# Optimization experiments

Measured on AMD Instinct MI355X. Metric: run time of the kernel, lower is better.

## Reference

```python
import jax, jax.numpy as jnp
import numpy as np


def setup_inputs() -> dict:
    key = jax.random.key(0)
    k1, k2 = jax.random.split(key)
    pred_corners = jax.random.normal(k1, (2048, 8, 3), dtype=jnp.float32)
    gt_corners = jax.random.normal(k2, (2048, 8, 3), dtype=jnp.float32)
    return {"pred_corners": pred_corners, "gt_corners": gt_corners}


def _chamfer(pred_corners, gt_corners):
    # flatten boxes -> point clouds: [Np*8, 3], [Ng*8, 3]
    x = pred_corners.reshape(-1, 3)
    y = gt_corners.reshape(-1, 3)
    x2 = jnp.sum(x * x, axis=-1)  # [N]
    y2 = jnp.sum(y * y, axis=-1)  # [M]
    d2 = x2[:, None] + y2[None, :] - 2.0 * jnp.einsum("nd,md->nm", x, y)
    dist = jnp.sqrt(jnp.maximum(d2, 0.0))  # [N, M]
    # bidirectional min, averaged per box (8 corners) then over boxes
    min_p2g = jnp.min(dist, axis=1).reshape(-1, 8).mean(axis=1)
    min_g2p = jnp.min(dist, axis=0).reshape(-1, 8).mean(axis=1)
    return min_p2g.mean() + min_g2p.mean()


def reference(pred_corners, gt_corners):
    return _chamfer(pred_corners, gt_corners)
```

## Files before the change

kernel.cpp:

```cpp
#include <hip/hip_runtime.h>


#define NPTS   16384
#define BLOCKB 512
#define WAVES  8
#define XT_W   8
#define XPB    (WAVES * XT_W * 16)
#define NXB    (NPTS / XPB)
#define NYCH   16
#define YCH    (NPTS / NYCH)
#define SUBT   8
#define SUBPTS (SUBT * 16)
#define NSUB   (YCH / SUBPTS)
#define ONEBF  0x3F80

#define WS_PGB (1u << 20)
#define WS_PGA (2u << 20)
#define WS_PPB (3u << 20)
#define WS_PART (4u << 20)

typedef __attribute__((ext_vector_type(8))) short bf16x8;
typedef __attribute__((ext_vector_type(4))) float f32x4;

__device__ inline unsigned short f2bf(float f) {
    unsigned int u = __float_as_uint(f);
    return (unsigned short)((u + 0x7FFFu + ((u >> 16) & 1u)) >> 16);
}
__device__ inline float bf2f(unsigned short h) {
    return __uint_as_float((unsigned int)h << 16);
}
__device__ inline void split3(float v, unsigned short* s) {
    unsigned short h = f2bf(v);  float r = v - bf2f(h);
    unsigned short m = f2bf(r);  r -= bf2f(m);
    s[0] = h; s[1] = m; s[2] = f2bf(r);
}

__device__ inline void build_rows(const float p[3], unsigned short* a,
                                  unsigned short* b) {
    const int CI[6] = {0, 0, 1, 0, 1, 2};
    const int CJ[6] = {0, 1, 0, 2, 1, 0};
    unsigned short xs[3][3], nn[3], t[3];
#pragma unroll
    for (int d = 0; d < 3; ++d) {
        split3(p[d], t);
        xs[0][d] = t[0]; xs[1][d] = t[1]; xs[2][d] = t[2];
    }
    split3(-0.5f * (p[0]*p[0] + p[1]*p[1] + p[2]*p[2]), nn);
#pragma unroll
    for (int c = 0; c < 6; ++c)
#pragma unroll
        for (int d = 0; d < 3; ++d) {
            a[c*3+d] = xs[CI[c]][d];
            b[c*3+d] = xs[CJ[c]][d];
        }
#pragma unroll
    for (int k = 0; k < 3; ++k) {
        a[18+k] = nn[k];  b[18+k] = ONEBF;
        a[21+k] = ONEBF;  b[21+k] = nn[k];
    }
#pragma unroll
    for (int k = 24; k < 32; ++k) { a[k] = 0; b[k] = 0; }
}

__device__ inline void store_row(unsigned short* dst, const unsigned short* s) {
    unsigned int w[16];
#pragma unroll
    for (int k = 0; k < 16; ++k)
        w[k] = (unsigned int)s[2*k] | ((unsigned int)s[2*k+1] << 16);
    uint4* d4 = reinterpret_cast<uint4*>(dst);
#pragma unroll
    for (int k = 0; k < 4; ++k)
        d4[k] = make_uint4(w[4*k], w[4*k+1], w[4*k+2], w[4*k+3]);
}

__global__ __launch_bounds__(256) void pack_points(
        const float* __restrict__ pred, const float* __restrict__ gt,
        unsigned short* __restrict__ Ppa, unsigned short* __restrict__ Pgb,
        unsigned short* __restrict__ Pga, unsigned short* __restrict__ Ppb) {
    const int i = blockIdx.x * 256 + threadIdx.x;
    if (i >= NPTS) return;
    float p[3] = {pred[3*i], pred[3*i+1], pred[3*i+2]};
    float q[3] = {gt[3*i],   gt[3*i+1],   gt[3*i+2]};
    unsigned short ra[32], rb[32];
    build_rows(p, ra, rb);
    store_row(Ppa + (size_t)i * 32, ra);
    store_row(Ppb + (size_t)i * 32, rb);
    build_rows(q, ra, rb);
    store_row(Pga + (size_t)i * 32, ra);
    store_row(Pgb + (size_t)i * 32, rb);
}

template <int CTRL>
__device__ inline float rormax(float v) {
    int t = __builtin_amdgcn_update_dpp(0, __float_as_int(v), CTRL, 0xF, 0xF,
                                        false);
    return fmaxf(v, __int_as_float(t));
}

__global__ __launch_bounds__(BLOCKB, 4) void chamfer_part(
        const unsigned short* __restrict__ Ppa,
        const unsigned short* __restrict__ Pgb,
        const unsigned short* __restrict__ Pga,
        const unsigned short* __restrict__ Ppb,
        float* __restrict__ part) {
    const int xb  = blockIdx.x;
    const int yc  = blockIdx.y;
    const int dir = blockIdx.z;
    const unsigned short* __restrict__ Ap = dir ? Pga : Ppa;
    const unsigned short* __restrict__ Bp = dir ? Ppb : Pgb;
    const int tid = threadIdx.x;
    const int lane = tid & 63, w = tid >> 6;
    const int col = lane & 15, kg = lane >> 4;

    __shared__ __align__(16) char lbuf[2][SUBT * 16 * 64];

    const int xt0 = xb * (WAVES * XT_W) + w * XT_W;
    bf16x8 af[XT_W];
#pragma unroll
    for (int xi = 0; xi < XT_W; ++xi)
        af[xi] = *reinterpret_cast<const bf16x8*>(
            Ap + (size_t)((xt0 + xi) * 16 + col) * 32 + kg * 8);

    f32x4 rmax[XT_W];
#pragma unroll
    for (int xi = 0; xi < XT_W; ++xi)
        rmax[xi] = (f32x4){-3.0e38f, -3.0e38f, -3.0e38f, -3.0e38f};

    const f32x4 z4 = {0.0f, 0.0f, 0.0f, 0.0f};
    const char* ysrc = reinterpret_cast<const char*>(Bp) + (size_t)yc * YCH * 64;

    uint4 ld = *reinterpret_cast<const uint4*>(ysrc + tid * 16);
#pragma unroll 1
    for (int sc = 0; sc < NSUB; ++sc) {
        __syncthreads();
        *reinterpret_cast<uint4*>(&lbuf[sc & 1][tid * 16]) = ld;
        if (sc + 1 < NSUB)
            ld = *reinterpret_cast<const uint4*>(
                ysrc + (size_t)(sc + 1) * (SUBPTS * 64) + tid * 16);
        __syncthreads();
        const char* buf = lbuf[sc & 1];
#pragma unroll
        for (int t = 0; t < SUBT; t += 2) {
            bf16x8 b0 = *reinterpret_cast<const bf16x8*>(
                buf + ((t + 0) * 16 + col) * 64 + kg * 16);
            bf16x8 b1 = *reinterpret_cast<const bf16x8*>(
                buf + ((t + 1) * 16 + col) * 64 + kg * 16);
#pragma unroll
            for (int xi = 0; xi < XT_W; ++xi) {
                f32x4 A = __builtin_amdgcn_mfma_f32_16x16x32_bf16(af[xi], b0, z4, 0, 0, 0);
                f32x4 B = __builtin_amdgcn_mfma_f32_16x16x32_bf16(af[xi], b1, z4, 0, 0, 0);
                rmax[xi].x = fmaxf(fmaxf(A.x, B.x), rmax[xi].x);
                rmax[xi].y = fmaxf(fmaxf(A.y, B.y), rmax[xi].y);
                rmax[xi].z = fmaxf(fmaxf(A.z, B.z), rmax[xi].z);
                rmax[xi].w = fmaxf(fmaxf(A.w, B.w), rmax[xi].w);
            }
        }
    }

    float* pslice = part + (size_t)(dir * NYCH + yc) * NPTS;
#pragma unroll
    for (int xi = 0; xi < XT_W; ++xi) {
#define FLUSH(R, COMP)                                                        \
        {                                                                     \
            float v = rmax[xi].COMP;                                          \
            v = rormax<0x121>(v);                                             \
            v = rormax<0x122>(v);                                             \
            v = rormax<0x124>(v);                                             \
            v = rormax<0x128>(v);                                             \
            if (col == 0) {                                                   \
                float d2 = fmaxf(-2.0f * v, 0.0f);           \
                pslice[(xt0 + xi) * 16 + kg * 4 + R] = d2;                    \
            }                                                                 \
        }
        FLUSH(0, x) FLUSH(1, y) FLUSH(2, z) FLUSH(3, w)
#undef FLUSH
    }
}

__global__ __launch_bounds__(256) void chamfer_reduce(
        const float* __restrict__ part, float* __restrict__ out) {
    const int gid = blockIdx.x * 256 + threadIdx.x;
    const int dir = gid >> 14, x = gid & (NPTS - 1);
    float m = 3.0e38f;
#pragma unroll
    for (int c = 0; c < NYCH; ++c)
        m = fminf(m, part[(size_t)(dir * NYCH + c) * NPTS + x]);
    float s = sqrtf(m);
#pragma unroll
    for (int off = 32; off > 0; off >>= 1)
        s += __shfl_down(s, off, 64);
    if ((threadIdx.x & 63) == 0)
        atomicAdd(out, s * (1.0f / (float)NPTS));
}

extern "C" void kernel_launch(void* const* d_in, const int* in_sizes, int n_in,
                              void* d_out, int out_size, void* d_ws, size_t ws_size,
                              hipStream_t stream) {
    const float* pred = (const float*)d_in[0];
    const float* gt   = (const float*)d_in[1];
    float* out        = (float*)d_out;
    unsigned short* Ppa = (unsigned short*)d_ws;
    unsigned short* Pgb = (unsigned short*)((char*)d_ws + WS_PGB);
    unsigned short* Pga = (unsigned short*)((char*)d_ws + WS_PGA);
    unsigned short* Ppb = (unsigned short*)((char*)d_ws + WS_PPB);
    float* part         = (float*)((char*)d_ws + WS_PART);

    hipMemsetAsync(d_out, 0, sizeof(float), stream);
    hipLaunchKernelGGL(pack_points, dim3(NPTS / 256), dim3(256), 0, stream,
                       pred, gt, Ppa, Pgb, Pga, Ppb);
    hipLaunchKernelGGL(chamfer_part, dim3(NXB, NYCH, 2), dim3(BLOCKB), 0, stream,
                       Ppa, Pgb, Pga, Ppb, part);
    hipLaunchKernelGGL(chamfer_reduce, dim3(2 * NPTS / 256), dim3(256), 0, stream,
                       part, out);
}
```

Before: 97.02 us.

## Compute both chamfer directions from one distance matrix pass

```diff
diff --git a/kernel.cpp b/kernel.cpp
--- a/kernel.cpp
+++ b/kernel.cpp
@@ -2,22 +2,16 @@
 
 
 #define NPTS   16384
-#define BLOCKB 512
-#define WAVES  8
-#define XT_W   8
-#define XPB    (WAVES * XT_W * 16)
-#define NXB    (NPTS / XPB)
-#define NYCH   16
-#define YCH    (NPTS / NYCH)
-#define SUBT   8
-#define SUBPTS (SUBT * 16)
-#define NSUB   (YCH / SUBPTS)
+#define BLOCK  256
+#define XCH    256
+#define NXC    (NPTS / XCH)
+#define YCH    1024
+#define NYC    (NPTS / YCH)
+#define YW     256
 #define ONEBF  0x3F80
 
-#define WS_PGB (1u << 20)
-#define WS_PGA (2u << 20)
-#define WS_PPB (3u << 20)
-#define WS_PART (4u << 20)
+#define WS_PGB  (1u << 20)
+#define WS_PART (2u << 20)
 
 typedef __attribute__((ext_vector_type(8))) short bf16x8;
 typedef __attribute__((ext_vector_type(4))) float f32x4;
@@ -75,8 +69,7 @@
 
 __global__ __launch_bounds__(256) void pack_points(
         const float* __restrict__ pred, const float* __restrict__ gt,
-        unsigned short* __restrict__ Ppa, unsigned short* __restrict__ Pgb,
-        unsigned short* __restrict__ Pga, unsigned short* __restrict__ Ppb) {
+        unsigned short* __restrict__ Ppa, unsigned short* __restrict__ Pgb) {
     const int i = blockIdx.x * 256 + threadIdx.x;
     if (i >= NPTS) return;
     float p[3] = {pred[3*i], pred[3*i+1], pred[3*i+2]};
@@ -84,9 +77,7 @@
     unsigned short ra[32], rb[32];
     build_rows(p, ra, rb);
     store_row(Ppa + (size_t)i * 32, ra);
-    store_row(Ppb + (size_t)i * 32, rb);
     build_rows(q, ra, rb);
-    store_row(Pga + (size_t)i * 32, ra);
     store_row(Pgb + (size_t)i * 32, rb);
 }
 
@@ -97,94 +88,87 @@
     return fmaxf(v, __int_as_float(t));
 }
 
-__global__ __launch_bounds__(BLOCKB, 4) void chamfer_part(
+__global__ __launch_bounds__(BLOCK, 4) void chamfer_bidi(
         const unsigned short* __restrict__ Ppa,
         const unsigned short* __restrict__ Pgb,
-        const unsigned short* __restrict__ Pga,
-        const unsigned short* __restrict__ Ppb,
         float* __restrict__ part) {
-    const int xb  = blockIdx.x;
-    const int yc  = blockIdx.y;
-    const int dir = blockIdx.z;
-    const unsigned short* __restrict__ Ap = dir ? Pga : Ppa;
-    const unsigned short* __restrict__ Bp = dir ? Ppb : Pgb;
-    const int tid = threadIdx.x;
-    const int lane = tid & 63, w = tid >> 6;
+    const int xb = blockIdx.x, yc = blockIdx.y;
+    const int lane = threadIdx.x & 63, w = threadIdx.x >> 6;
     const int col = lane & 15, kg = lane >> 4;
+    const int xbase = xb * XCH;
+    const int ybase = yc * YCH + w * YW;
 
-    __shared__ __align__(16) char lbuf[2][SUBT * 16 * 64];
+    float* __restrict__ rowp = part + (size_t)(yc * 4 + w) * NPTS;
+    float* __restrict__ colp = part + (size_t)(64 + xb) * NPTS;
 
-    const int xt0 = xb * (WAVES * XT_W) + w * XT_W;
-    bf16x8 af[XT_W];
+    bf16x8 bfr[16];
 #pragma unroll
-    for (int xi = 0; xi < XT_W; ++xi)
-        af[xi] = *reinterpret_cast<const bf16x8*>(
-            Ap + (size_t)((xt0 + xi) * 16 + col) * 32 + kg * 8);
+    for (int yt = 0; yt < 16; ++yt)
+        bfr[yt] = *reinterpret_cast<const bf16x8*>(
+            Pgb + (size_t)(ybase + yt * 16 + col) * 32 + kg * 8);
 
-    f32x4 rmax[XT_W];
+    float cmax[16];
 #pragma unroll
-    for (int xi = 0; xi < XT_W; ++xi)
-        rmax[xi] = (f32x4){-3.0e38f, -3.0e38f, -3.0e38f, -3.0e38f};
+    for (int yt = 0; yt < 16; ++yt) cmax[yt] = -3.0e38f;
 
     const f32x4 z4 = {0.0f, 0.0f, 0.0f, 0.0f};
-    const char* ysrc = reinterpret_cast<const char*>(Bp) + (size_t)yc * YCH * 64;
 
-    uint4 ld = *reinterpret_cast<const uint4*>(ysrc + tid * 16);
+    bf16x8 afn = *reinterpret_cast<const bf16x8*>(
+        Ppa + (size_t)(xbase + col) * 32 + kg * 8);
+
 #pragma unroll 1
-    for (int sc = 0; sc < NSUB; ++sc) {
-        __syncthreads();
-        *reinterpret_cast<uint4*>(&lbuf[sc & 1][tid * 16]) = ld;
-        if (sc + 1 < NSUB)
-            ld = *reinterpret_cast<const uint4*>(
-                ysrc + (size_t)(sc + 1) * (SUBPTS * 64) + tid * 16);
-        __syncthreads();
-        const char* buf = lbuf[sc & 1];
+    for (int xt = 0; xt < 16; ++xt) {
+        bf16x8 afc = afn;
+        afn = *reinterpret_cast<const bf16x8*>(
+            Ppa + (size_t)(xbase + (((xt + 1) & 15) * 16) + col) * 32 + kg * 8);
+
+        f32x4 rmax = {-3.0e38f, -3.0e38f, -3.0e38f, -3.0e38f};
 #pragma unroll
-        for (int t = 0; t < SUBT; t += 2) {
-            bf16x8 b0 = *reinterpret_cast<const bf16x8*>(
-                buf + ((t + 0) * 16 + col) * 64 + kg * 16);
-            bf16x8 b1 = *reinterpret_cast<const bf16x8*>(
-                buf + ((t + 1) * 16 + col) * 64 + kg * 16);
+        for (int yt = 0; yt < 16; yt += 2) {
+            f32x4 A = __builtin_amdgcn_mfma_f32_16x16x32_bf16(afc, bfr[yt],     z4, 0, 0, 0);
+            f32x4 B = __builtin_amdgcn_mfma_f32_16x16x32_bf16(afc, bfr[yt + 1], z4, 0, 0, 0);
+            rmax.x = fmaxf(fmaxf(A.x, B.x), rmax.x);
+            rmax.y = fmaxf(fmaxf(A.y, B.y), rmax.y);
+            rmax.z = fmaxf(fmaxf(A.z, B.z), rmax.z);
+            rmax.w = fmaxf(fmaxf(A.w, B.w), rmax.w);
+            float ta = fmaxf(fmaxf(A.x, A.y), A.z);
+            cmax[yt]     = fmaxf(fmaxf(ta, A.w), cmax[yt]);
+            float tb = fmaxf(fmaxf(B.x, B.y), B.z);
+            cmax[yt + 1] = fmaxf(fmaxf(tb, B.w), cmax[yt + 1]);
+        }
+
 #pragma unroll
-            for (int xi = 0; xi < XT_W; ++xi) {
-                f32x4 A = __builtin_amdgcn_mfma_f32_16x16x32_bf16(af[xi], b0, z4, 0, 0, 0);
-                f32x4 B = __builtin_amdgcn_mfma_f32_16x16x32_bf16(af[xi], b1, z4, 0, 0, 0);
-                rmax[xi].x = fmaxf(fmaxf(A.x, B.x), rmax[xi].x);
-                rmax[xi].y = fmaxf(fmaxf(A.y, B.y), rmax[xi].y);
-                rmax[xi].z = fmaxf(fmaxf(A.z, B.z), rmax[xi].z);
-                rmax[xi].w = fmaxf(fmaxf(A.w, B.w), rmax[xi].w);
-            }
+        for (int i = 0; i < 4; ++i) {
+            float v = rmax[i];
+            v = rormax<0x121>(v);
+            v = rormax<0x122>(v);
+            v = rormax<0x124>(v);
+            v = rormax<0x128>(v);
+            if (col == 0)
+                rowp[xbase + xt * 16 + kg * 4 + i] =
+                    fmaxf(-2.0f * v, 0.0f);
         }
     }
 
-    float* pslice = part + (size_t)(dir * NYCH + yc) * NPTS;
 #pragma unroll
-    for (int xi = 0; xi < XT_W; ++xi) {
-#define FLUSH(R, COMP)                                                        \
-        {                                                                     \
-            float v = rmax[xi].COMP;                                          \
-            v = rormax<0x121>(v);                                             \
-            v = rormax<0x122>(v);                                             \
-            v = rormax<0x124>(v);                                             \
-            v = rormax<0x128>(v);                                             \
-            if (col == 0) {                                                   \
-                float d2 = fmaxf(-2.0f * v, 0.0f);           \
-                pslice[(xt0 + xi) * 16 + kg * 4 + R] = d2;                    \
-            }                                                                 \
-        }
-        FLUSH(0, x) FLUSH(1, y) FLUSH(2, z) FLUSH(3, w)
-#undef FLUSH
+    for (int yt = 0; yt < 16; ++yt) {
+        float v = cmax[yt];
+        v = fmaxf(v, __shfl_xor(v, 16, 64));
+        v = fmaxf(v, __shfl_xor(v, 32, 64));
+        if (kg == 0)
+            colp[ybase + yt * 16 + col] = fmaxf(-2.0f * v, 0.0f);
     }
 }
 
 __global__ __launch_bounds__(256) void chamfer_reduce(
         const float* __restrict__ part, float* __restrict__ out) {
     const int gid = blockIdx.x * 256 + threadIdx.x;
-    const int dir = gid >> 14, x = gid & (NPTS - 1);
+    const int side = gid >> 14, idx = gid & (NPTS - 1);
+    const float* base = part + (size_t)side * 64 * NPTS + idx;
     float m = 3.0e38f;
-#pragma unroll
-    for (int c = 0; c < NYCH; ++c)
-        m = fminf(m, part[(size_t)(dir * NYCH + c) * NPTS + x]);
+#pragma unroll 8
+    for (int c = 0; c < 64; ++c)
+        m = fminf(m, base[(size_t)c * NPTS]);
     float s = sqrtf(m);
 #pragma unroll
     for (int off = 32; off > 0; off >>= 1)
@@ -201,15 +185,13 @@
     float* out        = (float*)d_out;
     unsigned short* Ppa = (unsigned short*)d_ws;
     unsigned short* Pgb = (unsigned short*)((char*)d_ws + WS_PGB);
-    unsigned short* Pga = (unsigned short*)((char*)d_ws + WS_PGA);
-    unsigned short* Ppb = (unsigned short*)((char*)d_ws + WS_PPB);
     float* part         = (float*)((char*)d_ws + WS_PART);
 
     hipMemsetAsync(d_out, 0, sizeof(float), stream);
     hipLaunchKernelGGL(pack_points, dim3(NPTS / 256), dim3(256), 0, stream,
-                       pred, gt, Ppa, Pgb, Pga, Ppb);
-    hipLaunchKernelGGL(chamfer_part, dim3(NXB, NYCH, 2), dim3(BLOCKB), 0, stream,
-                       Ppa, Pgb, Pga, Ppb, part);
+                       pred, gt, Ppa, Pgb);
+    hipLaunchKernelGGL(chamfer_bidi, dim3(NXC, NYC), dim3(BLOCK), 0, stream,
+                       Ppa, Pgb, part);
     hipLaunchKernelGGL(chamfer_reduce, dim3(2 * NPTS / 256), dim3(256), 0, stream,
                        part, out);
 }
```

New measurement: 152.4 us. 1.57x slower.
